# Performance work log

Measured on AMD Instinct MI355X. Metric: run time of the kernel, lower is better.

Reference implementation:

```python
import jax, jax.numpy as jnp
import numpy as np

N = 6000        # graph nodes
DEG = 16        # fixed out-degree -> 1-hop neighborhood size DEG+1
M = DEG + 1     # neighborhood size
NT = 16         # n_templates
MT = 10         # nodes per template
NF = 128        # node features
REG = 0.1       # entropic regularisation
N_ITER = 10     # mirror-descent iterations of the entropic semi-relaxed FGW solver


def setup_inputs() -> dict:
    key = jax.random.key(0)
    k1, k2, k3, k4 = jax.random.split(key, 4)
    x = jax.random.normal(k1, (N, NF), jnp.float32)
    dst = jax.random.randint(k2, (N * DEG,), 0, N, jnp.int32)
    src = jnp.repeat(jnp.arange(N, dtype=jnp.int32), DEG)
    edge_index = jnp.stack([src, dst])  # (2, N*DEG)
    # template_initialisation: symmetrized uniform adjacency + N(0, 0.001) features
    templates = jax.random.uniform(k3, (NT, MT, MT), jnp.float32)
    templates = 0.5 * (templates + templates.transpose(0, 2, 1))
    templates_features = 0.001 * jax.random.normal(k4, (NT, MT, NF), jnp.float32)
    alpha0 = jnp.zeros((1,), jnp.float32)  # nn.Parameter init; alpha = sigmoid(0) = 0.5
    return {"x": x, "edge_index": edge_index, "templates": templates,
            "templates_features": templates_features, "alpha0": alpha0}


def _srfgw_marginals(C1, F1, p, C2, F2, alpha):
    """Entropic semi-relaxed FGW (mirror descent, square loss) per (node, template).
    C1:(N,M,M) F1:(N,M,NF) p:(M,)  C2:(NT,MT,MT) F2:(NT,MT,NF)
    Returns second marginal q = T^T 1 of the optimal plan, shape (N,NT,MT)."""
    # squared-Euclidean feature cost  (N,NT,M,MT)
    Mcost = (jnp.sum(F1 ** 2, -1)[:, None, :, None]
             + jnp.sum(F2 ** 2, -1)[None, :, None, :]
             - 2.0 * jnp.einsum('nmf,ktf->nkmt', F1, F2))
    C2sq = C2 ** 2
    c1p = jnp.einsum('nab,b->na', C1 ** 2, p)  # (N,M) constant GW term
    # init plan T0 = p q0^T with uniform q0; work in log-domain for stability
    lt = jnp.broadcast_to(jnp.log(p)[None, None, :, None] - jnp.log(float(MT)),
                          Mcost.shape)

    def step(lt):
        T = p[None, None, :, None] * jax.nn.softmax(lt, axis=-1)  # rows sum to p
        q = T.sum(axis=2)                                         # (N,NT,MT)
        constC2 = jnp.einsum('nkb,kjb->nkj', q, C2sq)             # q-dependent GW term
        Y = jnp.einsum('nab,nkbt->nkat', C1, T)
        Y = jnp.einsum('nkat,kst->nkas', Y, C2)                   # C1 T C2^T
        gw_grad = 2.0 * (c1p[:, None, :, None] + constC2[:, :, None, :] - 2.0 * Y)
        grad = alpha * gw_grad + (1.0 - alpha) * Mcost
        # mirror step: T <- Proj_{T1=p} T*exp(-grad/reg)  (log-domain)
        return lt - grad / REG

    for _ in range(N_ITER):
        lt = step(lt)
    T = p[None, None, :, None] * jax.nn.softmax(lt, axis=-1)
    return T.sum(axis=2)


def reference(x, edge_index, templates, templates_features, alpha0):
    alpha = jax.nn.sigmoid(alpha0[0])
    src, dst = edge_index[0], edge_index[1]
    A = jnp.zeros((N, N), x.dtype).at[src, dst].set(1.0)
    A = jnp.maximum(A, A.T)  # undirected adjacency
    # 1-hop (k=1) neighborhood: node itself + its DEG out-neighbors
    nbrs = jnp.concatenate([jnp.arange(N, dtype=jnp.int32)[:, None],
                            dst.reshape(N, DEG)], axis=1)        # (N,M)
    C1 = A[nbrs[:, :, None], nbrs[:, None, :]]                   # (N,M,M) subgraph adj
    F1 = x[nbrs]                                                 # (N,M,NF)
    p = jnp.full((M,), 1.0 / M, x.dtype)                         # uniform node weights
    q = _srfgw_marginals(C1, F1, p, templates, templates_features, alpha)
    return q.reshape(N, NT * MT)  # per-node embedding: marginals to each template
```

## Files before the change

kernel.cpp:

```cpp
#include <hip/hip_runtime.h>


#define NN    6000
#define DEG   16
#define MM    17
#define NTPL  16
#define MT    10
#define NF    128
#define NITER 10
#define KPB   4
#define NPB   7
#define BS    512
#define RS    12
#define LOG2E 1.44269504088896340736f

template<int C>
__device__ __forceinline__ float ror_add(float v) {
    int s = __builtin_amdgcn_update_dpp(0, __float_as_int(v), C, 0xf, 0xf, true);
    return v + __int_as_float(s);
}

__device__ __forceinline__ float fexp2(float x) { return __builtin_amdgcn_exp2f(x); }
__device__ __forceinline__ float frcp(float x)  { return __builtin_amdgcn_rcpf(x); }

__device__ __forceinline__ float reduce16(float v) {
    v = ror_add<0x121>(v);
    v = ror_add<0x122>(v);
    v = ror_add<0x124>(v);
    v = ror_add<0x128>(v);
    return v;
}

#define GNV 40
__global__ __launch_bounds__(256) void gcost_kernel(
    const float* __restrict__ x, const float* __restrict__ F2g,
    const float* __restrict__ alpha0, float* __restrict__ G)
{
    const int kt  = blockIdx.y * 16 + (threadIdx.x >> 4);
    const int l16 = threadIdx.x & 15;

    const float4* f2p = reinterpret_cast<const float4*>(F2g + (size_t)kt * NF) + l16 * 2;
    const float4 f2a = f2p[0], f2b = f2p[1];
    float sq = reduce16(f2a.x * f2a.x + f2a.y * f2a.y + f2a.z * f2a.z + f2a.w * f2a.w
                      + f2b.x * f2b.x + f2b.y * f2b.y + f2b.z * f2b.z + f2b.w * f2b.w);

    const float alpha  = 1.f / (1.f + __expf(-alpha0[0]));
    const float mcoefl = (1.f - alpha) * 10.f * LOG2E;
    const float base   = mcoefl * sq;
    const float m2     = -2.f * mcoefl;

    const int v0 = blockIdx.x * GNV;
    #pragma unroll 4
    for (int i = 0; i < GNV; i++) {
        const int v = v0 + i;
        const float4* xp = reinterpret_cast<const float4*>(x + (size_t)v * NF) + l16 * 2;
        float4 xa = xp[0], xb = xp[1];
        float d = xa.x * f2a.x + xa.y * f2a.y + xa.z * f2a.z + xa.w * f2a.w
                + xb.x * f2b.x + xb.y * f2b.y + xb.z * f2b.z + xb.w * f2b.w;
        d = reduce16(d);
        if (l16 == 0)
            G[(size_t)v * (NTPL * MT) + kt] = fmaf(m2, d, base);
    }
}

__global__ __launch_bounds__(BS, 4) void srfgw_kernel(
    const float* __restrict__ x,
    const int*   __restrict__ dst,
    const float* __restrict__ C2g,
    const float* __restrict__ F2g,
    const float* __restrict__ alpha0,
    const float* __restrict__ G,
    int useG,
    float*       __restrict__ out)
{
    const int nb  = blockIdx.x * NPB;
    const int kb  = blockIdx.y * KPB;
    const int tid = threadIdx.x;

    __shared__ __align__(16) float s_T[KPB][NPB][MM][RS];
    __shared__ __align__(16) float s_C2sq[KPB][MT][RS];
    __shared__ __align__(16) float s_q[KPB][NPB][RS];
    __shared__ __align__(16) float s_cc[KPB][NPB][RS];
    __shared__ __align__(16) float s_A[KPB][RS];
    __shared__ __align__(16) float s_B[KPB][RS];
    __shared__ __align__(16) int   s_adj[NPB * MM][DEG];
    __shared__ int      s_nbr[NPB][MM];
    __shared__ unsigned s_mask[NPB][MM];

    const float aval  = alpha0[0];
    const float alpha = 1.f / (1.f + __expf(-aval));
    const float gcoef = 2.f * alpha * 10.f;
    const float tgl   = 2.f * gcoef * LOG2E;
    const float gl2   = gcoef * LOG2E;

    if (tid < NPB * MM) {
        int node = tid / MM, a0 = tid - node * MM;
        int nd  = nb + node;
        int ndc = nd < NN ? nd : NN - 1;
        s_nbr[node][a0]  = (a0 == 0) ? ndc : dst[(size_t)ndc * DEG + a0 - 1];
        s_mask[node][a0] = 0u;
    }
    __syncthreads();

    for (int i = tid; i < NPB * MM * DEG; i += BS) {
        int r = i >> 4, j = i & 15;
        int node = r / MM, a0 = r - node * MM;
        s_adj[r][j] = dst[(size_t)s_nbr[node][a0] * DEG + j];
    }
    for (int i = tid; i < KPB * MT * MT; i += BS) {
        int kk = i / (MT * MT), rr = i - kk * (MT * MT);
        int rs = rr / MT, rt = rr - rs * MT;
        float v = C2g[(size_t)kb * MT * MT + i];
        s_C2sq[kk][rs][rt] = gl2 * v * v;
    }
    if (tid < KPB * MT) {
        int kk = tid / MT, s = tid - kk * MT;
        const float* cr = C2g + (size_t)(kb + kk) * MT * MT + s * MT;
        float rs = 0.f, rq = 0.f;
        #pragma unroll
        for (int t = 0; t < MT; t++) { float c = cr[t]; rs += c; rq = fmaf(c, c, rq); }
        s_A[kk][s] = (tgl / 170.f) * rs;
        s_B[kk][s] = 0.1f * gl2 * rq;
    }
    __syncthreads();

    for (int i = tid; i < NPB * MM * MM; i += BS) {
        int node = i / (MM * MM), rr = i - node * (MM * MM);
        int pa = rr / MM, pb = rr - pa * MM;
        int vtgt = s_nbr[node][pb];
        const int* ar = s_adj[node * MM + pa];
        bool e = false;
        #pragma unroll
        for (int j = 0; j < DEG; j++) e = e | (ar[j] == vtgt);
        if (e) {
            atomicOr(&s_mask[node][pa], 1u << pb);
            atomicOr(&s_mask[node][pb], 1u << pa);
        }
    }
    __syncthreads();

    const int  kh     = tid >> 7;
    const int  L      = tid & 127;
    const bool rvalid = L < NPB * MM;
    int gR = L / MM;
    int aR = L - gR * MM;
    if (!rvalid) { gR = 0; aR = 0; }

    const int k_u = __builtin_amdgcn_readfirstlane(kb + kh);
    const float* __restrict__ c2p = C2g + (size_t)k_u * MT * MT;

    const int vv = s_nbr[gR][aR];

    float Mc[MT];
    if (useG) {
        const float2* gp = reinterpret_cast<const float2*>(G + (size_t)vv * (NTPL * MT) + k_u * MT);
        #pragma unroll
        for (int j = 0; j < 5; j++) {
            float2 w = gp[j];
            Mc[2 * j] = w.x; Mc[2 * j + 1] = w.y;
        }
    } else {
        float dot[MT], sq2[MT];
        #pragma unroll
        for (int t = 0; t < MT; t++) { dot[t] = 0.f; sq2[t] = 0.f; }
        const float4* xr = reinterpret_cast<const float4*>(x + (size_t)vv * NF);
        const float4* fr = reinterpret_cast<const float4*>(F2g + (size_t)k_u * MT * NF);
        for (int f = 0; f < NF / 4; f++) {
            float4 xa = xr[f];
            #pragma unroll
            for (int t = 0; t < MT; t++) {
                float4 b = fr[t * (NF / 4) + f];
                dot[t] += xa.x * b.x + xa.y * b.y + xa.z * b.z + xa.w * b.w;
                sq2[t] += b.x * b.x + b.y * b.y + b.z * b.z + b.w * b.w;
            }
        }
        const float mcoefl = (1.f - alpha) * 10.f * LOG2E;
        #pragma unroll
        for (int t = 0; t < MT; t++) Mc[t] = mcoefl * (sq2[t] - 2.f * dot[t]);
    }

    unsigned mask = rvalid ? s_mask[gR][aR] : 0u;
    const int  pcnt = __popc(mask);
    const bool cmpl = pcnt > 8;
    unsigned   lmask = cmpl ? (~mask & 0x1FFFFu) : mask;
    if (!rvalid) lmask = 0u;
    const float sgn = cmpl ? -1.f : 1.f;
    const float P   = 1.f / 17.f;

    float lt[MT];
    {
        const float pcf = (float)pcnt;
        const float2* Ap = reinterpret_cast<const float2*>(&s_A[kh][0]);
        const float2* Bp = reinterpret_cast<const float2*>(&s_B[kh][0]);
        #pragma unroll
        for (int j = 0; j < 5; j++) {
            float2 av = Ap[j], bv = Bp[j];
            lt[2 * j]     = fmaf(pcf, av.x, -bv.x - Mc[2 * j]);
            lt[2 * j + 1] = fmaf(pcf, av.y, -bv.y - Mc[2 * j + 1]);
        }
    }

    const bool cvalid = tid < KPB * NPB * MT;
    int ck = 0, cn = 0, ct = 0;
    if (cvalid) {
        ck = tid / (NPB * MT);
        int rem = tid - ck * (NPB * MT);
        cn = rem / MT;
        ct = rem - cn * MT;
    }
    float qa = 0.f;

    float4* Trow = reinterpret_cast<float4*>(&s_T[kh][gR][aR][0]);

    for (int it = 1; it <= NITER; it++) {
        float mx = lt[0];
        #pragma unroll
        for (int t = 1; t < MT; t++) mx = fmaxf(mx, lt[t]);
        float e[MT], ss = 0.f;
        #pragma unroll
        for (int t = 0; t < MT; t++) { e[t] = fexp2(lt[t] - mx); ss += e[t]; }
        float sc = P * frcp(ss);
        #pragma unroll
        for (int t = 0; t < MT; t++) e[t] *= sc;

        if (rvalid) {
            Trow[0] = make_float4(e[0], e[1], e[2], e[3]);
            Trow[1] = make_float4(e[4], e[5], e[6], e[7]);
            reinterpret_cast<float2*>(Trow)[4] = make_float2(e[8], e[9]);
        }
        __syncthreads();

        if (cvalid) {
            const float* colp = &s_T[ck][cn][0][ct];
            float s0 = 0.f;
            #pragma unroll
            for (int m = 0; m < MM; m++) s0 += colp[m * RS];
            qa = s0;
            s_q[ck][cn][ct] = s0;
        }
        __syncthreads();
        if (it == NITER) break;

        if (cvalid) {
            const float4* qp4 = reinterpret_cast<const float4*>(&s_q[ck][cn][0]);
            float4 qx = qp4[0], qy = qp4[1];
            float2 qz = reinterpret_cast<const float2*>(qp4)[4];
            const float4* cr = reinterpret_cast<const float4*>(&s_C2sq[ck][ct][0]);
            float4 ca = cr[0], cb = cr[1];
            float2 c2 = reinterpret_cast<const float2*>(cr)[4];
            float cc = qx.x * ca.x + qx.y * ca.y + qx.z * ca.z + qx.w * ca.w
                     + qy.x * cb.x + qy.y * cb.y + qy.z * cb.z + qy.w * cb.w
                     + qz.x * c2.x + qz.y * c2.y;
            s_cc[ck][cn][ct] = cc;
        }

        float q[MT];
        {
            const float4* qp4 = reinterpret_cast<const float4*>(&s_q[kh][gR][0]);
            float4 qx = qp4[0], qy = qp4[1];
            float2 qz = reinterpret_cast<const float2*>(qp4)[4];
            q[0] = qx.x; q[1] = qx.y; q[2] = qx.z; q[3] = qx.w;
            q[4] = qy.x; q[5] = qy.y; q[6] = qy.z; q[7] = qy.w;
            q[8] = qz.x; q[9] = qz.y;
        }
        float y1[MT];
        #pragma unroll
        for (int t = 0; t < MT; t++) y1[t] = cmpl ? q[t] : 0.f;
        unsigned mm = lmask;
        while (mm) {
            int b = __ffs(mm) - 1;
            mm &= mm - 1;
            const float4* rb4 = reinterpret_cast<const float4*>(&s_T[kh][gR][b][0]);
            float4 ra = rb4[0], rb = rb4[1];
            float2 rc = reinterpret_cast<const float2*>(rb4)[4];
            y1[0] += sgn * ra.x; y1[1] += sgn * ra.y; y1[2] += sgn * ra.z; y1[3] += sgn * ra.w;
            y1[4] += sgn * rb.x; y1[5] += sgn * rb.y; y1[6] += sgn * rb.z; y1[7] += sgn * rb.w;
            y1[8] += sgn * rc.x; y1[9] += sgn * rc.y;
        }
        #pragma unroll
        for (int s = 0; s < MT; s++) {
            float y2 = 0.f;
            #pragma unroll
            for (int t = 0; t < MT; t++) y2 = fmaf(y1[t], c2p[s * MT + t], y2);
            lt[s] += tgl * y2 - Mc[s];
        }
        __syncthreads();

        {
            const float4* cp = reinterpret_cast<const float4*>(&s_cc[kh][gR][0]);
            float4 ca = cp[0], cb = cp[1];
            float2 c2 = reinterpret_cast<const float2*>(cp)[4];
            lt[0] -= ca.x; lt[1] -= ca.y; lt[2] -= ca.z; lt[3] -= ca.w;
            lt[4] -= cb.x; lt[5] -= cb.y; lt[6] -= cb.z; lt[7] -= cb.w;
            lt[8] -= c2.x; lt[9] -= c2.y;
        }
    }

    if (cvalid) {
        int nOut = nb + cn;
        if (nOut < NN)
            out[(size_t)nOut * (NTPL * MT) + (kb + ck) * MT + ct] = qa;
    }
}

extern "C" void kernel_launch(void* const* d_in, const int* in_sizes, int n_in,
                              void* d_out, int out_size, void* d_ws, size_t ws_size,
                              hipStream_t stream) {
    const float* x      = (const float*)d_in[0];
    const int*   eidx   = (const int*)d_in[1];
    const float* tmpl   = (const float*)d_in[2];
    const float* tmplf  = (const float*)d_in[3];
    const float* alpha0 = (const float*)d_in[4];
    float*       outp   = (float*)d_out;

    const int* dst = eidx + NN * DEG;
    float* G = (float*)d_ws;
    const size_t gbytes = (size_t)NN * NTPL * MT * sizeof(float);
    int useG = (ws_size >= gbytes) ? 1 : 0;

    if (useG)
        gcost_kernel<<<dim3(NN / GNV, 10), dim3(256), 0, stream>>>(x, tmplf, alpha0, G);

    srfgw_kernel<<<dim3((NN + NPB - 1) / NPB, NTPL / KPB), dim3(BS), 0, stream>>>(
        x, dst, tmpl, tmplf, alpha0, G, useG, outp);
}
```

Baseline: 202.9 us.

## Rewrite feature-cost precompute as shared-memory tiled register-blocked GEMM

The cost-matrix precompute kernel used a 16-lane dot product with DPP reductions per (node, template-node) pair and re-read x from global for every pair. It now stages 64 node rows and 32 template rows in LDS and computes a 4x4 register tile of dot products per thread, which gives reuse of x and F2 across outputs. Template squared norms are computed once per block through shared partial sums. Output stores are strided per thread, and the LDS footprint per block is larger.

```diff
diff --git a/kernel.cpp b/kernel.cpp
--- a/kernel.cpp
+++ b/kernel.cpp
@@ -14,52 +14,96 @@
 #define RS    12
 #define LOG2E 1.44269504088896340736f
 
-template<int C>
-__device__ __forceinline__ float ror_add(float v) {
-    int s = __builtin_amdgcn_update_dpp(0, __float_as_int(v), C, 0xf, 0xf, true);
-    return v + __int_as_float(s);
-}
-
 __device__ __forceinline__ float fexp2(float x) { return __builtin_amdgcn_exp2f(x); }
 __device__ __forceinline__ float frcp(float x)  { return __builtin_amdgcn_rcpf(x); }
 
-__device__ __forceinline__ float reduce16(float v) {
-    v = ror_add<0x121>(v);
-    v = ror_add<0x122>(v);
-    v = ror_add<0x124>(v);
-    v = ror_add<0x128>(v);
-    return v;
-}
-
-#define GNV 40
-__global__ __launch_bounds__(256) void gcost_kernel(
+#define GBN  64
+#define GBK  32
+#define GPAD 132
+
+__global__ __launch_bounds__(128) void gcost_kernel(
     const float* __restrict__ x, const float* __restrict__ F2g,
     const float* __restrict__ alpha0, float* __restrict__ G)
 {
-    const int kt  = blockIdx.y * 16 + (threadIdx.x >> 4);
-    const int l16 = threadIdx.x & 15;
-
-    const float4* f2p = reinterpret_cast<const float4*>(F2g + (size_t)kt * NF) + l16 * 2;
-    const float4 f2a = f2p[0], f2b = f2p[1];
-    float sq = reduce16(f2a.x * f2a.x + f2a.y * f2a.y + f2a.z * f2a.z + f2a.w * f2a.w
-                      + f2b.x * f2b.x + f2b.y * f2b.y + f2b.z * f2b.z + f2b.w * f2b.w);
+    __shared__ __align__(16) float xs[GBN][GPAD];
+    __shared__ __align__(16) float fs[GBK][GPAD];
+    __shared__ float ps[GBK][4];
+
+    const int tid = threadIdx.x;
+    const int n0  = blockIdx.x * GBN;
+    const int k0  = blockIdx.y * GBK;
+
+    for (int i = tid; i < GBN * 32; i += 128) {
+        int r = i >> 5, c = i & 31;
+        int v = n0 + r; if (v >= NN) v = NN - 1;
+        float4 w = reinterpret_cast<const float4*>(x + (size_t)v * NF)[c];
+        *reinterpret_cast<float4*>(&xs[r][c * 4]) = w;
+    }
+    for (int i = tid; i < GBK * 32; i += 128) {
+        int r = i >> 5, c = i & 31;
+        float4 w = reinterpret_cast<const float4*>(F2g + (size_t)(k0 + r) * NF)[c];
+        *reinterpret_cast<float4*>(&fs[r][c * 4]) = w;
+    }
+    __syncthreads();
+
+    {
+        int r = tid & 31, q = tid >> 5;
+        const float4* fp = reinterpret_cast<const float4*>(&fs[r][q * 32]);
+        float s = 0.f;
+        #pragma unroll
+        for (int c = 0; c < 8; c++) {
+            float4 w = fp[c];
+            s += w.x * w.x + w.y * w.y + w.z * w.z + w.w * w.w;
+        }
+        ps[r][q] = s;
+    }
+    __syncthreads();
+
+    const int jk = tid & 7;
+    const int nn = tid >> 3;
+
+    float acc[4][4];
+    #pragma unroll
+    for (int c = 0; c < 4; c++)
+        #pragma unroll
+        for (int t = 0; t < 4; t++) acc[c][t] = 0.f;
+
+    #pragma unroll 4
+    for (int f = 0; f < NF / 4; f++) {
+        float4 xa[4], fb[4];
+        #pragma unroll
+        for (int c = 0; c < 4; c++)
+            xa[c] = *reinterpret_cast<const float4*>(&xs[nn + 16 * c][f * 4]);
+        #pragma unroll
+        for (int t = 0; t < 4; t++)
+            fb[t] = *reinterpret_cast<const float4*>(&fs[jk + 8 * t][f * 4]);
+        #pragma unroll
+        for (int c = 0; c < 4; c++)
+            #pragma unroll
+            for (int t = 0; t < 4; t++) {
+                acc[c][t] = fmaf(xa[c].x, fb[t].x, acc[c][t]);
+                acc[c][t] = fmaf(xa[c].y, fb[t].y, acc[c][t]);
+                acc[c][t] = fmaf(xa[c].z, fb[t].z, acc[c][t]);
+                acc[c][t] = fmaf(xa[c].w, fb[t].w, acc[c][t]);
+            }
+    }
 
     const float alpha  = 1.f / (1.f + __expf(-alpha0[0]));
     const float mcoefl = (1.f - alpha) * 10.f * LOG2E;
-    const float base   = mcoefl * sq;
     const float m2     = -2.f * mcoefl;
 
-    const int v0 = blockIdx.x * GNV;
-    #pragma unroll 4
-    for (int i = 0; i < GNV; i++) {
-        const int v = v0 + i;
-        const float4* xp = reinterpret_cast<const float4*>(x + (size_t)v * NF) + l16 * 2;
-        float4 xa = xp[0], xb = xp[1];
-        float d = xa.x * f2a.x + xa.y * f2a.y + xa.z * f2a.z + xa.w * f2a.w
-                + xb.x * f2b.x + xb.y * f2b.y + xb.z * f2b.z + xb.w * f2b.w;
-        d = reduce16(d);
-        if (l16 == 0)
-            G[(size_t)v * (NTPL * MT) + kt] = fmaf(m2, d, base);
+    #pragma unroll
+    for (int t = 0; t < 4; t++) {
+        int krow = jk + 8 * t;
+        float sq   = ps[krow][0] + ps[krow][1] + ps[krow][2] + ps[krow][3];
+        float base = mcoefl * sq;
+        int   kt   = k0 + krow;
+        #pragma unroll
+        for (int c = 0; c < 4; c++) {
+            int v = n0 + nn + 16 * c;
+            if (v < NN)
+                G[(size_t)v * (NTPL * MT) + kt] = fmaf(m2, acc[c][t], base);
+        }
     }
 }
 
@@ -319,7 +363,8 @@
     int useG = (ws_size >= gbytes) ? 1 : 0;
 
     if (useG)
-        gcost_kernel<<<dim3(NN / GNV, 10), dim3(256), 0, stream>>>(x, tmplf, alpha0, G);
+        gcost_kernel<<<dim3((NN + GBN - 1) / GBN, NTPL * MT / GBK), dim3(128), 0, stream>>>(
+            x, tmplf, alpha0, G);
 
     srfgw_kernel<<<dim3((NN + NPB - 1) / NPB, NTPL / KPB), dim3(BS), 0, stream>>>(
         x, dst, tmpl, tmplf, alpha0, G, useG, outp);
```

Result: no change. 201.7 us (-0.6%).
